# Optimization experiments

Measured on AMD Instinct MI355X. Metric: run time of the kernel, lower is better.

Reference implementation:

```python
import jax, jax.numpy as jnp
from jax import lax
import numpy as np

CONF_THR = 1e-4   # confidence_threshold
NMS_THR = 0.5     # nms_threshold


def haar2d(x):
    # x: [N, H, W] -> LL, LH, HL, HH each [N, H//2, W//2] (single-level Haar DWT)
    a = x[:, 0::2, 0::2]
    b = x[:, 0::2, 1::2]
    c = x[:, 1::2, 0::2]
    d = x[:, 1::2, 1::2]
    LL = (a + b + c + d) * 0.5
    LH = (a + b - c - d) * 0.5
    HL = (a - b + c - d) * 0.5
    HH = (a - b - c + d) * 0.5
    return LL, LH, HL, HH


def nms_keep(boxes, masked_scores, valid, nms_thr):
    # Greedy NMS, faithful to the torch while-loop: process in descending score
    # order; a box is kept iff not suppressed by an earlier kept box with IoU > thr.
    N = boxes.shape[0]
    order = jnp.argsort(-masked_scores)
    b = boxes[order]
    v = valid[order]
    x1, y1, x2, y2 = b[:, 0], b[:, 1], b[:, 2], b[:, 3]
    areas = (x2 - x1) * (y2 - y1)
    idx = jnp.arange(N)

    def body(i, st):
        sup, keep = st
        cur = jnp.logical_and(jnp.logical_not(sup[i]), v[i])
        keep = keep.at[i].set(cur)
        xx1 = jnp.maximum(x1, x1[i])
        yy1 = jnp.maximum(y1, y1[i])
        xx2 = jnp.minimum(x2, x2[i])
        yy2 = jnp.minimum(y2, y2[i])
        inter = jnp.maximum(xx2 - xx1, 0.0) * jnp.maximum(yy2 - yy1, 0.0)
        iou = inter / (areas[i] + areas - inter)
        sup = sup | (cur & (iou > nms_thr) & (idx > i))
        return sup, keep

    sup0 = jnp.logical_not(v)  # invalid boxes never kept
    keep0 = jnp.zeros((N,), dtype=bool)
    _, keep_sorted = lax.fori_loop(0, N, body, (sup0, keep0))
    # map back to original box order
    return jnp.zeros((N,), dtype=bool).at[order].set(keep_sorted)


def reference(boxes, scores, logits, features, labels):
    N = boxes.shape[0]
    # wavelet decomposition of per-detection feature maps
    LL, LH, HL, HH = haar2d(features)

    # detection quality = confidence * max softmax prob * box geometry quality
    max_prob = jnp.max(jax.nn.softmax(logits, axis=-1), axis=-1)
    w = boxes[:, 2] - boxes[:, 0]
    h = boxes[:, 3] - boxes[:, 1]
    aspect = jnp.minimum(w / h, h / w)
    area = w * h
    area_score = jnp.clip(area / (jnp.max(area) + 1e-6), 0.0, 1.0)
    det_quality = scores * max_prob * (aspect * area_score)

    # feature quality: feature bank is empty at init -> ones (exact initial-state semantics)
    feat_quality = jnp.ones((N,), dtype=boxes.dtype)

    # edge quality from high-frequency subbands (mean |.| over flattened subband dim)
    h_edge = jnp.mean(jnp.abs(LH.reshape(N, -1)), axis=1)
    v_edge = jnp.mean(jnp.abs(HL.reshape(N, -1)), axis=1)
    d_edge = jnp.mean(jnp.abs(HH.reshape(N, -1)), axis=1)
    edge_quality = (h_edge + v_edge + d_edge) / 3.0

    quality = det_quality * 0.4 + feat_quality * 0.3 + edge_quality * 0.3

    valid = quality > CONF_THR
    masked_scores = jnp.where(valid, scores, -jnp.inf)
    keep = nms_keep(lax.stop_gradient(boxes), lax.stop_gradient(masked_scores), valid, NMS_THR)

    # fixed-shape output: [N,6] = (boxes, score, quality) zeroed where not kept
    out = jnp.concatenate([boxes, scores[:, None], quality[:, None]], axis=1)
    out = out * keep[:, None].astype(out.dtype)
    return out, keep, labels


def setup_inputs() -> dict:
    key = jax.random.key(0)
    k1, k2, k3, k4, k5, k6 = jax.random.split(key, 6)
    N, C, H, W = 8192, 1000, 64, 64
    cxcy = jax.random.uniform(k1, (N, 2), dtype=jnp.float32) * 1000.0
    wh = jax.random.uniform(k2, (N, 2), dtype=jnp.float32) * 100.0 + 1.0
    boxes = jnp.concatenate([cxcy - wh / 2, cxcy + wh / 2], axis=1)
    scores = jax.random.uniform(k3, (N,), dtype=jnp.float32)
    logits = jax.random.normal(k4, (N, C), dtype=jnp.float32) * 3.0
    features = jax.random.normal(k5, (N, H, W), dtype=jnp.float32)
    labels = jax.random.randint(k6, (N,), 0, C)
    return {"boxes": boxes, "scores": scores, "logits": logits, "features": features, "labels": labels}
```

## Files before the change

### kernel.cpp

```cpp
#include <hip/hip_runtime.h>

#pragma clang fp contract(off)

typedef unsigned long long u64;
typedef unsigned int u32;
typedef float f32x4 __attribute__((ext_vector_type(4)));

#define NB 8192
#define NW 128
#define EMAX 16384
#define ELDS 12288

#define OFF_EDGEQ 0
#define OFF_MP    (OFF_EDGEQ + NB * 4)
#define OFF_KEEP  (OFF_MP    + NB * 4)
#define OFF_ECNT  (OFF_KEEP  + NW * 8)
#define OFF_MAXA  (OFF_ECNT  + 64)
#define OFF_EDGES (OFF_MAXA  + 192)

__device__ __forceinline__ float4 ldnt4(const float4* p) {
    f32x4 v = __builtin_nontemporal_load((const f32x4*)p);
    return make_float4(v.x, v.y, v.z, v.w);
}

__device__ __forceinline__ float haar3(float a, float b, float c, float d) {
    return fabsf(a + b - c - d) + fabsf(a - b + c - d) + fabsf(a - b - c + d);
}

__global__ __launch_bounds__(256) void k_edge(const float* __restrict__ feat,
                                              float* __restrict__ edgeq,
                                              u32* __restrict__ ecnt,
                                              u32* __restrict__ maxab) {
    int n = blockIdx.x;
    int t = threadIdx.x;
    if (n == 0 && t == 0) { *ecnt = 0; *maxab = 0; }
    const float* f = feat + (size_t)n * 4096;
    int hr = t >> 3, g = t & 7;
    const float4* row0 = (const float4*)(f + (2 * hr) * 64);
    const float4* row1 = (const float4*)(f + (2 * hr) * 64 + 64);
    float4 e0 = ldnt4(row0 + g);
    float4 e1 = ldnt4(row0 + 8 + g);
    float4 o0 = ldnt4(row1 + g);
    float4 o1 = ldnt4(row1 + 8 + g);
    float s = haar3(e0.x, e0.y, o0.x, o0.y) + haar3(e0.z, e0.w, o0.z, o0.w)
            + haar3(e1.x, e1.y, o1.x, o1.y) + haar3(e1.z, e1.w, o1.z, o1.w);
    for (int off = 32; off; off >>= 1) s += __shfl_down(s, off, 64);
    __shared__ float wsum[4];
    int wv = t >> 6, ln = t & 63;
    if (ln == 0) wsum[wv] = s;
    __syncthreads();
    if (t == 0) edgeq[n] = (wsum[0] + wsum[1] + wsum[2] + wsum[3]) * (0.5f / 3072.0f);
}

__global__ __launch_bounds__(256) void k_logit(const float* __restrict__ logits,
                                               float* __restrict__ mp) {
    int wave = threadIdx.x >> 6, lane = threadIdx.x & 63;
    int row = blockIdx.x * 4 + wave;
    const float4* p = (const float4*)(logits + (size_t)row * 1000);
    float4 v0 = ldnt4(p + lane);
    float4 v1 = ldnt4(p + lane + 64);
    float4 v2 = ldnt4(p + lane + 128);
    bool has3 = (lane + 192) < 250;
    float4 v3 = ldnt4(p + (has3 ? (lane + 192) : lane));
    float m = fmaxf(fmaxf(fmaxf(v0.x, v0.y), fmaxf(v0.z, v0.w)),
                    fmaxf(fmaxf(v1.x, v1.y), fmaxf(v1.z, v1.w)));
    m = fmaxf(m, fmaxf(fmaxf(v2.x, v2.y), fmaxf(v2.z, v2.w)));
    if (has3) m = fmaxf(m, fmaxf(fmaxf(v3.x, v3.y), fmaxf(v3.z, v3.w)));
    for (int off = 32; off; off >>= 1) m = fmaxf(m, __shfl_xor(m, off, 64));
    float s = __expf(v0.x - m) + __expf(v0.y - m) + __expf(v0.z - m) + __expf(v0.w - m)
            + __expf(v1.x - m) + __expf(v1.y - m) + __expf(v1.z - m) + __expf(v1.w - m)
            + __expf(v2.x - m) + __expf(v2.y - m) + __expf(v2.z - m) + __expf(v2.w - m);
    if (has3) s += __expf(v3.x - m) + __expf(v3.y - m) + __expf(v3.z - m) + __expf(v3.w - m);
    for (int off = 32; off; off >>= 1) s += __shfl_xor(s, off, 64);
    if (lane == 0) mp[row] = 1.0f / s;
}

__global__ __launch_bounds__(256) void k_mat(const float* __restrict__ boxes,
        const float* __restrict__ scores, u32* __restrict__ ecnt,
        u32* __restrict__ edges, u32* __restrict__ maxab) {
    int it = blockIdx.y;
    if ((int)blockIdx.x * 4 + 3 < it) return;
    int wv = threadIdx.x >> 6, lane = threadIdx.x & 63;
    int jt = blockIdx.x * 4 + wv;
    bool active = (jt >= it);
    __shared__ float sh[4][6][64];
    if (active) {
        int j0 = jt * 64;
        float4 bj = ((const float4*)boxes)[j0 + lane];
        sh[wv][0][lane] = bj.x; sh[wv][1][lane] = bj.y;
        sh[wv][2][lane] = bj.z; sh[wv][3][lane] = bj.w;
        sh[wv][4][lane] = (bj.z - bj.x) * (bj.w - bj.y);
        sh[wv][5][lane] = scores[j0 + lane];
    }
    __syncthreads();
    if (!active) return;
    int j0 = jt * 64;
    int i = it * 64 + lane;
    float4 bi = ((const float4*)boxes)[i];
    float X1 = bi.x, Y1 = bi.y, X2 = bi.z, Y2 = bi.w;
    float AR = (bi.z - bi.x) * (bi.w - bi.y);
    float SI = scores[i];
    bool diag = (jt == it);
    if (diag) {
        float am = AR;
        for (int off = 32; off; off >>= 1) am = fmaxf(am, __shfl_xor(am, off, 64));
        if (lane == 0) atomicMax(maxab, __float_as_uint(am));
    }
    #pragma unroll 4
    for (int b = 0; b < 64; ++b) {
        if (diag && b <= lane) continue;
        float xx1 = fmaxf(sh[wv][0][b], X1);
        float yy1 = fmaxf(sh[wv][1][b], Y1);
        float xx2 = fminf(sh[wv][2][b], X2);
        float yy2 = fminf(sh[wv][3][b], Y2);
        float iw = fmaxf(xx2 - xx1, 0.0f);
        float ih = fmaxf(yy2 - yy1, 0.0f);
        float inter = iw * ih;
        float denom = (AR + sh[wv][4][b]) - inter;
        if (inter > 0.25f * denom) {
            float iou = inter / denom;
            if (iou > 0.5f) {
                int j = j0 + b;
                float SJ = sh[wv][5][b];
                bool ihi = (SI > SJ) || (SI == SJ && i < j);
                u32 hi = ihi ? (u32)i : (u32)j;
                u32 lo = ihi ? (u32)j : (u32)i;
                u32 pos = atomicAdd(ecnt, 1u);
                if (pos < EMAX) edges[pos] = (hi << 16) | lo;
            }
        }
    }
}

__global__ __launch_bounds__(256) void k_scan4(const u32* __restrict__ ecnt,
        const u32* __restrict__ edges, u64* __restrict__ keepm) {
    __shared__ u64 dec[NW], kept[NW], keptIn[NW], pendIn[NW];
    __shared__ u32 eL[ELDS];
    __shared__ int undec;
    int tid = threadIdx.x;
    int E = (int)min(*ecnt, (u32)EMAX);
    if (tid < NW) { dec[tid] = 0; kept[tid] = 0; }
    for (int e = tid; e < E && e < ELDS; e += 256) eL[e] = edges[e];
    __syncthreads();
    for (int round = 0; round < NB; ++round) {
        if (tid < NW) { keptIn[tid] = 0; pendIn[tid] = 0; }
        if (tid == 0) undec = 0;
        __syncthreads();
        for (int e = tid; e < E; e += 256) {
            u32 pk = (e < ELDS) ? eL[e] : edges[e];
            int hi = (int)(pk >> 16), lo = (int)(pk & 0xFFFFu);
            bool d = (dec[hi >> 6] >> (hi & 63)) & 1ull;
            bool k = (kept[hi >> 6] >> (hi & 63)) & 1ull;
            if (!d)     atomicOr(&pendIn[lo >> 6], 1ull << (lo & 63));
            else if (k) atomicOr(&keptIn[lo >> 6], 1ull << (lo & 63));
        }
        __syncthreads();
        if (tid < NW) {
            u64 und = ~dec[tid];
            u64 sup = und & keptIn[tid];
            u64 kp  = und & ~keptIn[tid] & ~pendIn[tid];
            kept[tid] |= kp;
            dec[tid]  |= sup | kp;
            if (und & ~(sup | kp)) undec = 1;
        }
        __syncthreads();
        if (!undec) break;
    }
    if (tid < NW) keepm[tid] = kept[tid];
}

__global__ __launch_bounds__(256) void k_out(const float* __restrict__ boxes,
        const float* __restrict__ scores, const float* __restrict__ edgeq,
        const float* __restrict__ mp, const u32* __restrict__ maxab,
        const u64* __restrict__ keepmask, const int* __restrict__ labels,
        float* __restrict__ out) {
    int n = blockIdx.x * 256 + threadIdx.x;
    bool kept = (keepmask[n >> 6] >> (n & 63)) & 1ull;
    float kf = kept ? 1.0f : 0.0f;
    float4 b = ((const float4*)boxes)[n];
    float w = b.z - b.x, h = b.w - b.y;
    float area = w * h;
    float aspect = fminf(w / h, h / w);
    float maxA = __uint_as_float(*maxab);
    float ascore = area / (maxA + 1e-6f);
    ascore = fminf(fmaxf(ascore, 0.f), 1.f);
    float sc = scores[n];
    float det = sc * mp[n] * (aspect * ascore);
    float q = det * 0.4f + 0.3f + edgeq[n] * 0.3f;
    float* o = out + (size_t)n * 6;
    o[0] = b.x * kf; o[1] = b.y * kf; o[2] = b.z * kf; o[3] = b.w * kf;
    o[4] = sc * kf;
    o[5] = q * kf;
    out[6 * NB + n] = kf;
    out[7 * NB + n] = (float)labels[n];
}

extern "C" void kernel_launch(void* const* d_in, const int* in_sizes, int n_in,
                              void* d_out, int out_size, void* d_ws, size_t ws_size,
                              hipStream_t stream) {
    const float* boxes  = (const float*)d_in[0];
    const float* scores = (const float*)d_in[1];
    const float* logits = (const float*)d_in[2];
    const float* feats  = (const float*)d_in[3];
    const int*   labels = (const int*)d_in[4];
    float* out = (float*)d_out;
    char* ws = (char*)d_ws;

    float* edgeq  = (float*)(ws + OFF_EDGEQ);
    float* mp     = (float*)(ws + OFF_MP);
    u64*   keepm  = (u64*)(ws + OFF_KEEP);
    u32*   ecnt   = (u32*)(ws + OFF_ECNT);
    u32*   maxab  = (u32*)(ws + OFF_MAXA);
    u32*   edges  = (u32*)(ws + OFF_EDGES);

    k_edge<<<NB, 256, 0, stream>>>(feats, edgeq, ecnt, maxab);
    k_logit<<<NB / 4, 256, 0, stream>>>(logits, mp);
    dim3 gmat(32, NW);
    k_mat<<<gmat, 256, 0, stream>>>(boxes, scores, ecnt, edges, maxab);
    k_scan4<<<1, 256, 0, stream>>>(ecnt, edges, keepm);
    k_out<<<NB / 256, 256, 0, stream>>>(boxes, scores, edgeq, mp, maxab, keepm, labels, out);
}
```

Before: 116.5 us.

## Fuse edge, logit and IoU kernels into one launch with per-block edge buffers

```diff
diff --git a/kernel.cpp b/kernel.cpp
--- a/kernel.cpp
+++ b/kernel.cpp
@@ -8,15 +8,20 @@
 
 #define NB 8192
 #define NW 128
-#define EMAX 16384
+#define NTILE 128
+#define NEDGEB 8192
+#define NLOGB 2048
+#define NMATB 4096
+#define CAPB 128
 #define ELDS 12288
 
 #define OFF_EDGEQ 0
 #define OFF_MP    (OFF_EDGEQ + NB * 4)
 #define OFF_KEEP  (OFF_MP    + NB * 4)
-#define OFF_ECNT  (OFF_KEEP  + NW * 8)
-#define OFF_MAXA  (OFF_ECNT  + 64)
-#define OFF_EDGES (OFF_MAXA  + 192)
+#define OFF_MAXPT (OFF_KEEP  + NW * 8)
+#define OFF_MAXA  (OFF_MAXPT + NTILE * 4)
+#define OFF_CNTB  (OFF_MAXA  + 256)
+#define OFF_EDGEB (OFF_CNTB  + NMATB * 4)
 
 __device__ __forceinline__ float4 ldnt4(const float4* p) {
     f32x4 v = __builtin_nontemporal_load((const f32x4*)p);
@@ -27,127 +32,146 @@
     return fabsf(a + b - c - d) + fabsf(a - b + c - d) + fabsf(a - b - c + d);
 }
 
-__global__ __launch_bounds__(256) void k_edge(const float* __restrict__ feat,
-                                              float* __restrict__ edgeq,
-                                              u32* __restrict__ ecnt,
-                                              u32* __restrict__ maxab) {
-    int n = blockIdx.x;
+__global__ __launch_bounds__(256) void k_front(const float* __restrict__ feat,
+        const float* __restrict__ boxes, const float* __restrict__ scores,
+        const float* __restrict__ logits, float* __restrict__ edgeq,
+        float* __restrict__ mp, float* __restrict__ maxPT,
+        u32* __restrict__ cntB, u32* __restrict__ edgesB) {
+    __shared__ float sh[4][6][64];
+    __shared__ u32 lcnt;
+    __shared__ u32 lbuf[CAPB];
+    __shared__ float wsum[4];
+    int bid = blockIdx.x;
     int t = threadIdx.x;
-    if (n == 0 && t == 0) { *ecnt = 0; *maxab = 0; }
-    const float* f = feat + (size_t)n * 4096;
-    int hr = t >> 3, g = t & 7;
-    const float4* row0 = (const float4*)(f + (2 * hr) * 64);
-    const float4* row1 = (const float4*)(f + (2 * hr) * 64 + 64);
-    float4 e0 = ldnt4(row0 + g);
-    float4 e1 = ldnt4(row0 + 8 + g);
-    float4 o0 = ldnt4(row1 + g);
-    float4 o1 = ldnt4(row1 + 8 + g);
-    float s = haar3(e0.x, e0.y, o0.x, o0.y) + haar3(e0.z, e0.w, o0.z, o0.w)
-            + haar3(e1.x, e1.y, o1.x, o1.y) + haar3(e1.z, e1.w, o1.z, o1.w);
-    for (int off = 32; off; off >>= 1) s += __shfl_down(s, off, 64);
-    __shared__ float wsum[4];
-    int wv = t >> 6, ln = t & 63;
-    if (ln == 0) wsum[wv] = s;
-    __syncthreads();
-    if (t == 0) edgeq[n] = (wsum[0] + wsum[1] + wsum[2] + wsum[3]) * (0.5f / 3072.0f);
-}
-
-__global__ __launch_bounds__(256) void k_logit(const float* __restrict__ logits,
-                                               float* __restrict__ mp) {
-    int wave = threadIdx.x >> 6, lane = threadIdx.x & 63;
-    int row = blockIdx.x * 4 + wave;
-    const float4* p = (const float4*)(logits + (size_t)row * 1000);
-    float4 v0 = ldnt4(p + lane);
-    float4 v1 = ldnt4(p + lane + 64);
-    float4 v2 = ldnt4(p + lane + 128);
-    bool has3 = (lane + 192) < 250;
-    float4 v3 = ldnt4(p + (has3 ? (lane + 192) : lane));
-    float m = fmaxf(fmaxf(fmaxf(v0.x, v0.y), fmaxf(v0.z, v0.w)),
-                    fmaxf(fmaxf(v1.x, v1.y), fmaxf(v1.z, v1.w)));
-    m = fmaxf(m, fmaxf(fmaxf(v2.x, v2.y), fmaxf(v2.z, v2.w)));
-    if (has3) m = fmaxf(m, fmaxf(fmaxf(v3.x, v3.y), fmaxf(v3.z, v3.w)));
-    for (int off = 32; off; off >>= 1) m = fmaxf(m, __shfl_xor(m, off, 64));
-    float s = __expf(v0.x - m) + __expf(v0.y - m) + __expf(v0.z - m) + __expf(v0.w - m)
-            + __expf(v1.x - m) + __expf(v1.y - m) + __expf(v1.z - m) + __expf(v1.w - m)
-            + __expf(v2.x - m) + __expf(v2.y - m) + __expf(v2.z - m) + __expf(v2.w - m);
-    if (has3) s += __expf(v3.x - m) + __expf(v3.y - m) + __expf(v3.z - m) + __expf(v3.w - m);
-    for (int off = 32; off; off >>= 1) s += __shfl_xor(s, off, 64);
-    if (lane == 0) mp[row] = 1.0f / s;
-}
-
-__global__ __launch_bounds__(256) void k_mat(const float* __restrict__ boxes,
-        const float* __restrict__ scores, u32* __restrict__ ecnt,
-        u32* __restrict__ edges, u32* __restrict__ maxab) {
-    int it = blockIdx.y;
-    if ((int)blockIdx.x * 4 + 3 < it) return;
-    int wv = threadIdx.x >> 6, lane = threadIdx.x & 63;
-    int jt = blockIdx.x * 4 + wv;
-    bool active = (jt >= it);
-    __shared__ float sh[4][6][64];
-    if (active) {
+    int wv = t >> 6, lane = t & 63;
+
+    if (bid < NEDGEB) {
+        int n = bid;
+        const float* f = feat + (size_t)n * 4096;
+        int hr = t >> 3, g = t & 7;
+        const float4* row0 = (const float4*)(f + (2 * hr) * 64);
+        const float4* row1 = (const float4*)(f + (2 * hr) * 64 + 64);
+        float4 e0 = ldnt4(row0 + g);
+        float4 e1 = ldnt4(row0 + 8 + g);
+        float4 o0 = ldnt4(row1 + g);
+        float4 o1 = ldnt4(row1 + 8 + g);
+        float s = haar3(e0.x, e0.y, o0.x, o0.y) + haar3(e0.z, e0.w, o0.z, o0.w)
+                + haar3(e1.x, e1.y, o1.x, o1.y) + haar3(e1.z, e1.w, o1.z, o1.w);
+        for (int off = 32; off; off >>= 1) s += __shfl_down(s, off, 64);
+        if (lane == 0) wsum[wv] = s;
+        __syncthreads();
+        if (t == 0) edgeq[n] = (wsum[0] + wsum[1] + wsum[2] + wsum[3]) * (0.5f / 3072.0f);
+    } else if (bid < NEDGEB + NLOGB) {
+        int row = (bid - NEDGEB) * 4 + wv;
+        const float4* p = (const float4*)(logits + (size_t)row * 1000);
+        float4 v0 = ldnt4(p + lane);
+        float4 v1 = ldnt4(p + lane + 64);
+        float4 v2 = ldnt4(p + lane + 128);
+        bool has3 = (lane + 192) < 250;
+        float4 v3 = ldnt4(p + (has3 ? (lane + 192) : lane));
+        float m = fmaxf(fmaxf(fmaxf(v0.x, v0.y), fmaxf(v0.z, v0.w)),
+                        fmaxf(fmaxf(v1.x, v1.y), fmaxf(v1.z, v1.w)));
+        m = fmaxf(m, fmaxf(fmaxf(v2.x, v2.y), fmaxf(v2.z, v2.w)));
+        if (has3) m = fmaxf(m, fmaxf(fmaxf(v3.x, v3.y), fmaxf(v3.z, v3.w)));
+        for (int off = 32; off; off >>= 1) m = fmaxf(m, __shfl_xor(m, off, 64));
+        float s = __expf(v0.x - m) + __expf(v0.y - m) + __expf(v0.z - m) + __expf(v0.w - m)
+                + __expf(v1.x - m) + __expf(v1.y - m) + __expf(v1.z - m) + __expf(v1.w - m)
+                + __expf(v2.x - m) + __expf(v2.y - m) + __expf(v2.z - m) + __expf(v2.w - m);
+        if (has3) s += __expf(v3.x - m) + __expf(v3.y - m) + __expf(v3.z - m) + __expf(v3.w - m);
+        for (int off = 32; off; off >>= 1) s += __shfl_xor(s, off, 64);
+        if (lane == 0) mp[row] = 1.0f / s;
+    } else {
+        int lin = bid - (NEDGEB + NLOGB);
+        int it = lin >> 5;
+        int jt = (lin & 31) * 4 + wv;
+        bool dead = ((lin & 31) * 4 + 3) < it;
+        bool active = !dead && (jt >= it);
+        if (t == 0) lcnt = 0;
         int j0 = jt * 64;
-        float4 bj = ((const float4*)boxes)[j0 + lane];
-        sh[wv][0][lane] = bj.x; sh[wv][1][lane] = bj.y;
-        sh[wv][2][lane] = bj.z; sh[wv][3][lane] = bj.w;
-        sh[wv][4][lane] = (bj.z - bj.x) * (bj.w - bj.y);
-        sh[wv][5][lane] = scores[j0 + lane];
-    }
-    __syncthreads();
-    if (!active) return;
-    int j0 = jt * 64;
-    int i = it * 64 + lane;
-    float4 bi = ((const float4*)boxes)[i];
-    float X1 = bi.x, Y1 = bi.y, X2 = bi.z, Y2 = bi.w;
-    float AR = (bi.z - bi.x) * (bi.w - bi.y);
-    float SI = scores[i];
-    bool diag = (jt == it);
-    if (diag) {
-        float am = AR;
-        for (int off = 32; off; off >>= 1) am = fmaxf(am, __shfl_xor(am, off, 64));
-        if (lane == 0) atomicMax(maxab, __float_as_uint(am));
-    }
-    #pragma unroll 4
-    for (int b = 0; b < 64; ++b) {
-        if (diag && b <= lane) continue;
-        float xx1 = fmaxf(sh[wv][0][b], X1);
-        float yy1 = fmaxf(sh[wv][1][b], Y1);
-        float xx2 = fminf(sh[wv][2][b], X2);
-        float yy2 = fminf(sh[wv][3][b], Y2);
-        float iw = fmaxf(xx2 - xx1, 0.0f);
-        float ih = fmaxf(yy2 - yy1, 0.0f);
-        float inter = iw * ih;
-        float denom = (AR + sh[wv][4][b]) - inter;
-        if (inter > 0.25f * denom) {
-            float iou = inter / denom;
-            if (iou > 0.5f) {
-                int j = j0 + b;
-                float SJ = sh[wv][5][b];
-                bool ihi = (SI > SJ) || (SI == SJ && i < j);
-                u32 hi = ihi ? (u32)i : (u32)j;
-                u32 lo = ihi ? (u32)j : (u32)i;
-                u32 pos = atomicAdd(ecnt, 1u);
-                if (pos < EMAX) edges[pos] = (hi << 16) | lo;
+        if (active) {
+            float4 bj = ((const float4*)boxes)[j0 + lane];
+            sh[wv][0][lane] = bj.x; sh[wv][1][lane] = bj.y;
+            sh[wv][2][lane] = bj.z; sh[wv][3][lane] = bj.w;
+            sh[wv][4][lane] = (bj.z - bj.x) * (bj.w - bj.y);
+            sh[wv][5][lane] = scores[j0 + lane];
+        }
+        __syncthreads();
+        if (active) {
+            int i = it * 64 + lane;
+            float4 bi = ((const float4*)boxes)[i];
+            float X1 = bi.x, Y1 = bi.y, X2 = bi.z, Y2 = bi.w;
+            float AR = (bi.z - bi.x) * (bi.w - bi.y);
+            float SI = scores[i];
+            bool diag = (jt == it);
+            if (diag) {
+                float am = AR;
+                for (int off = 32; off; off >>= 1) am = fmaxf(am, __shfl_xor(am, off, 64));
+                if (lane == 0) maxPT[it] = am;
             }
-        }
-    }
-}
-
-__global__ __launch_bounds__(256) void k_scan4(const u32* __restrict__ ecnt,
-        const u32* __restrict__ edges, u64* __restrict__ keepm) {
+            #pragma unroll 4
+            for (int b = 0; b < 64; ++b) {
+                if (diag && b <= lane) continue;
+                float xx1 = fmaxf(sh[wv][0][b], X1);
+                float yy1 = fmaxf(sh[wv][1][b], Y1);
+                float xx2 = fminf(sh[wv][2][b], X2);
+                float yy2 = fminf(sh[wv][3][b], Y2);
+                float iw = fmaxf(xx2 - xx1, 0.0f);
+                float ih = fmaxf(yy2 - yy1, 0.0f);
+                float inter = iw * ih;
+                float denom = (AR + sh[wv][4][b]) - inter;
+                if (inter > 0.25f * denom) {
+                    float iou = inter / denom;
+                    if (iou > 0.5f) {
+                        int j = j0 + b;
+                        float SJ = sh[wv][5][b];
+                        bool ihi = (SI > SJ) || (SI == SJ && i < j);
+                        u32 hi = ihi ? (u32)i : (u32)j;
+                        u32 lo = ihi ? (u32)j : (u32)i;
+                        u32 pos = atomicAdd(&lcnt, 1u);
+                        if (pos < CAPB) lbuf[pos] = (hi << 16) | lo;
+                    }
+                }
+            }
+        }
+        __syncthreads();
+        u32 c = min(lcnt, (u32)CAPB);
+        if (t == 0) cntB[lin] = c;
+        for (u32 e = t; e < c; e += 256) edgesB[(size_t)lin * CAPB + e] = lbuf[e];
+    }
+}
+
+__global__ __launch_bounds__(256) void k_scan5(const u32* __restrict__ cntB,
+        const u32* __restrict__ edgesB, const float* __restrict__ maxPT,
+        float* __restrict__ maxab, u64* __restrict__ keepm) {
     __shared__ u64 dec[NW], kept[NW], keptIn[NW], pendIn[NW];
     __shared__ u32 eL[ELDS];
+    __shared__ u32 gcnt;
     __shared__ int undec;
     int tid = threadIdx.x;
-    int E = (int)min(*ecnt, (u32)EMAX);
+    if (tid < 64) {
+        float v = fmaxf(maxPT[tid], maxPT[tid + 64]);
+        for (int off = 32; off; off >>= 1) v = fmaxf(v, __shfl_xor(v, off, 64));
+        if (tid == 0) *maxab = v;
+    }
     if (tid < NW) { dec[tid] = 0; kept[tid] = 0; }
-    for (int e = tid; e < E && e < ELDS; e += 256) eL[e] = edges[e];
+    if (tid == 0) gcnt = 0;
     __syncthreads();
+    for (int b = tid; b < NMATB; b += 256) {
+        u32 c = cntB[b];
+        if (c) {
+            u32 base = atomicAdd(&gcnt, c);
+            for (u32 e = 0; e < c; ++e)
+                if (base + e < ELDS) eL[base + e] = edgesB[(size_t)b * CAPB + e];
+        }
+    }
+    __syncthreads();
+    int E = (int)min(gcnt, (u32)ELDS);
     for (int round = 0; round < NB; ++round) {
         if (tid < NW) { keptIn[tid] = 0; pendIn[tid] = 0; }
         if (tid == 0) undec = 0;
         __syncthreads();
         for (int e = tid; e < E; e += 256) {
-            u32 pk = (e < ELDS) ? eL[e] : edges[e];
+            u32 pk = eL[e];
             int hi = (int)(pk >> 16), lo = (int)(pk & 0xFFFFu);
             bool d = (dec[hi >> 6] >> (hi & 63)) & 1ull;
             bool k = (kept[hi >> 6] >> (hi & 63)) & 1ull;
@@ -171,7 +195,7 @@
 
 __global__ __launch_bounds__(256) void k_out(const float* __restrict__ boxes,
         const float* __restrict__ scores, const float* __restrict__ edgeq,
-        const float* __restrict__ mp, const u32* __restrict__ maxab,
+        const float* __restrict__ mp, const float* __restrict__ maxab,
         const u64* __restrict__ keepmask, const int* __restrict__ labels,
         float* __restrict__ out) {
     int n = blockIdx.x * 256 + threadIdx.x;
@@ -181,7 +205,7 @@
     float w = b.z - b.x, h = b.w - b.y;
     float area = w * h;
     float aspect = fminf(w / h, h / w);
-    float maxA = __uint_as_float(*maxab);
+    float maxA = *maxab;
     float ascore = area / (maxA + 1e-6f);
     ascore = fminf(fmaxf(ascore, 0.f), 1.f);
     float sc = scores[n];
@@ -209,14 +233,13 @@
     float* edgeq  = (float*)(ws + OFF_EDGEQ);
     float* mp     = (float*)(ws + OFF_MP);
     u64*   keepm  = (u64*)(ws + OFF_KEEP);
-    u32*   ecnt   = (u32*)(ws + OFF_ECNT);
-    u32*   maxab  = (u32*)(ws + OFF_MAXA);
-    u32*   edges  = (u32*)(ws + OFF_EDGES);
-
-    k_edge<<<NB, 256, 0, stream>>>(feats, edgeq, ecnt, maxab);
-    k_logit<<<NB / 4, 256, 0, stream>>>(logits, mp);
-    dim3 gmat(32, NW);
-    k_mat<<<gmat, 256, 0, stream>>>(boxes, scores, ecnt, edges, maxab);
-    k_scan4<<<1, 256, 0, stream>>>(ecnt, edges, keepm);
+    float* maxPT  = (float*)(ws + OFF_MAXPT);
+    float* maxab  = (float*)(ws + OFF_MAXA);
+    u32*   cntB   = (u32*)(ws + OFF_CNTB);
+    u32*   edgesB = (u32*)(ws + OFF_EDGEB);
+
+    k_front<<<NEDGEB + NLOGB + NMATB, 256, 0, stream>>>(feats, boxes, scores, logits,
+                                                        edgeq, mp, maxPT, cntB, edgesB);
+    k_scan5<<<1, 256, 0, stream>>>(cntB, edgesB, maxPT, maxab, keepm);
     k_out<<<NB / 256, 256, 0, stream>>>(boxes, scores, edgeq, mp, maxab, keepm, labels, out);
 }
```

Measured after the change: 131.2 us. 1.13x slower.
